# Optimization experiments

Hardware: AMD Instinct MI355X
Metric: run time of the kernel (lower is better)

Reference implementation:

```python
import jax, jax.numpy as jnp
import numpy as np

B, S, HID = 2, 2048, 1024
NH = 16
HD = HID // NH  # 64
ROPE_BASE = 10000.0
NEG_INF = -1e9


def _rope_emb(seq_len):
    # emb = cat(sin, cos) over head_dim, shape [1, S, 1, HD]
    inv_freq = 1.0 / (ROPE_BASE ** (jnp.arange(0, HD, 2, dtype=jnp.float32) / HD))
    pos = jnp.arange(seq_len, dtype=jnp.float32)
    sincos = pos[:, None] * inv_freq[None, :]            # [S, HD/2]
    emb = jnp.concatenate([jnp.sin(sincos), jnp.cos(sincos)], axis=-1)  # [S, HD]
    return emb[None, :, None, :]


def _apply_rope(x, emb):
    # Faithful to the (quirky) torch code: cos = emb[..., 1::2], sin = emb[..., ::2]
    cos = emb[..., 1::2]
    sin = emb[..., ::2]
    xe = x[..., ::2]
    xo = x[..., 1::2]
    return jnp.concatenate([xe * cos - xo * sin, xe * sin + xo * cos], axis=-1)


def setup_inputs() -> dict:
    key = jax.random.key(0)
    ks = jax.random.split(key, 5)
    hidden_states = jax.random.normal(ks[0], (B, S, HID), dtype=jnp.float32)
    # causal additive mask, broadcast over batch/heads
    causal = jnp.tril(jnp.ones((S, S), dtype=bool))
    attention_mask = jnp.where(causal, 0.0, NEG_INF).astype(jnp.float32)[None, None]
    scale = 1.0 / np.sqrt(HID)
    w_q = jax.random.normal(ks[1], (HID, HID), dtype=jnp.float32) * scale
    w_k = jax.random.normal(ks[2], (HID, HID), dtype=jnp.float32) * scale
    w_v = jax.random.normal(ks[3], (HID, HID), dtype=jnp.float32) * scale
    w_o = jax.random.normal(ks[4], (HID, HID), dtype=jnp.float32) * scale
    return {"hidden_states": hidden_states, "attention_mask": attention_mask,
            "w_q": w_q, "w_k": w_k, "w_v": w_v, "w_o": w_o}


def reference(hidden_states, attention_mask, w_q, w_k, w_v, w_o):
    b, s, _ = hidden_states.shape
    # torch Linear: x @ W.T (W is [out, in])
    q = (hidden_states @ w_q.T).reshape(b, s, NH, HD)
    k = (hidden_states @ w_k.T).reshape(b, s, NH, HD)
    v = (hidden_states @ w_v.T).reshape(b, s, NH, HD)
    emb = _rope_emb(s)
    q = _apply_rope(q, emb)
    k = _apply_rope(k, emb)
    # [b, h, s, d]
    q = q.transpose(0, 2, 1, 3)
    k = k.transpose(0, 2, 1, 3)
    v = v.transpose(0, 2, 1, 3)
    scores = jnp.einsum('bhqd,bhkd->bhqk', q, k) / np.sqrt(HD)
    scores = scores + attention_mask
    attn = jax.nn.softmax(scores, axis=-1)
    out = jnp.einsum('bhqk,bhkd->bhqd', attn, v)
    out = out.transpose(0, 2, 1, 3).reshape(b, s, HID)
    return out @ w_o.T
```

## Files before the change

### kernel.cpp

```cpp
#include <hip/hip_runtime.h>
#include <hip/hip_bf16.h>
#include <math.h>

typedef unsigned short u16;
typedef unsigned int   u32;
typedef unsigned long long u64;
typedef __attribute__((ext_vector_type(8))) short bf16x8;
typedef __attribute__((ext_vector_type(4))) short bf16x4;
typedef __attribute__((ext_vector_type(4))) float f32x4;

#define B_   2
#define S_   2048
#define HID_ 1024
#define NH_  16
#define HD_  64
#define MR_  (B_*S_)

#define QSCALE 0.1803368801111137f
#define MBIAS 32.0f

__device__ __forceinline__ u16 f2bf(float f) {
  union { float f; u32 u; } x; x.f = f;
  u32 r = x.u + 0x7fffu + ((x.u >> 16) & 1u);
  return (u16)(r >> 16);
}
__device__ __forceinline__ void gload16(const void* g, void* l) {
  __builtin_amdgcn_global_load_lds(
      (const __attribute__((address_space(1))) u32*)g,
      (__attribute__((address_space(3))) u32*)l, 16, 0, 0);
}

__global__ void k_cvt_all(const float* __restrict__ hs, const float* __restrict__ wq,
                          const float* __restrict__ wk, const float* __restrict__ wv,
                          const float* __restrict__ wo, ushort4* __restrict__ dst) {
  int i = blockIdx.x * blockDim.x + threadIdx.x;
  const float4* src;
  int idx;
  if (i < 1048576) {
    src = (const float4*)hs; idx = i;
  } else {
    int j = i - 1048576;
    int w = j >> 18; idx = j & 262143;
    src = (const float4*)(w == 0 ? wq : w == 1 ? wk : w == 2 ? wv : wo);
  }
  float4 v = src[idx];
  ushort4 o;
  o.x = f2bf(v.x); o.y = f2bf(v.y); o.z = f2bf(v.z); o.w = f2bf(v.w);
  dst[i] = o;
}

__global__ void k_rope_table(float2* __restrict__ tab) {
  int t = blockIdx.x * blockDim.x + threadIdx.x;
  int p = t >> 5, j = t & 31;
  double fp = (double)p;
  double c, s;
  if (j < 16) {
    s = sin(fp * pow(10000.0, -(2.0 * j) / 32.0));
    c = sin(fp * pow(10000.0, -(2.0 * j + 1.0) / 32.0));
  } else {
    s = cos(fp * pow(10000.0, -(2.0 * j - 32.0) / 32.0));
    c = cos(fp * pow(10000.0, -(2.0 * j - 31.0) / 32.0));
  }
  tab[p * 32 + j] = make_float2((float)c, (float)s);
}

__global__ __launch_bounds__(256) void k_qkv4(
    const u16* __restrict__ A,
    const u16* __restrict__ W0, const u16* __restrict__ W1, const u16* __restrict__ W2,
    u16* __restrict__ O0, u16* __restrict__ O1, u16* __restrict__ O2,
    const float2* __restrict__ tab) {
  __shared__ __align__(16) u16 Alds[2][2][128 * 32];
  __shared__ __align__(16) u16 Blds[2][2][128 * 32];

  int tid = threadIdx.x;
  int lane = tid & 63, wave = tid >> 6;
  int m0 = blockIdx.y * 128;
  int nt0 = blockIdx.x * 128;
  int wi = nt0 >> 10;
  const u16* W = (wi == 0) ? W0 : (wi == 1 ? W1 : W2);
  int n0 = nt0 & 1023;
  int wm = wave >> 1, wn = wave & 1;
  int lg = lane >> 4, lr = lane & 15;

  f32x4 acc[4][4];
  const f32x4 vz = {0.f, 0.f, 0.f, 0.f};
#pragma unroll
  for (int i = 0; i < 4; ++i)
#pragma unroll
    for (int j = 0; j < 4; ++j) acc[i][j] = vz;

  auto SA = [&](int j_, int d_, int hk_) {
#pragma unroll
    for (int it = 0; it < 2; ++it) {
      int c = it * 256 + tid;
      int row = c >> 2, sl = c & 3;
      int cw = sl ^ ((row >> 1) & 3);
      gload16(&A[(size_t)(m0 + row) * HID_ + j_ * 64 + hk_ * 32 + cw * 8],
              &Alds[d_][hk_][(it * 256 + wave * 64) * 8]);
    }
  };
  auto SB = [&](int j_, int d_, int hk_) {
#pragma unroll
    for (int it = 0; it < 2; ++it) {
      int c = it * 256 + tid;
      int row = c >> 2, sl = c & 3;
      int cw = sl ^ ((row >> 1) & 3);
      gload16(&W[(size_t)(n0 + row) * HID_ + j_ * 64 + hk_ * 32 + cw * 8],
              &Blds[d_][hk_][(it * 256 + wave * 64) * 8]);
    }
  };

  SA(0, 0, 0); SB(0, 0, 0); SA(0, 0, 1); SB(0, 0, 1);

  for (int j = 0; j < 16; ++j) {
    int cur = j & 1, nxt = cur ^ 1;
    bool more = (j < 15);
    bf16x8 bfr[4], afr[2];

    asm volatile("s_waitcnt vmcnt(4)" ::: "memory");
    __builtin_amdgcn_s_barrier();
    __builtin_amdgcn_sched_barrier(0);
    if (more) SA(j + 1, nxt, 0);
#pragma unroll
    for (int ni = 0; ni < 4; ++ni) {
      int row = wn * 64 + ni * 16 + lr;
      int ci = lg ^ ((row >> 1) & 3);
      bfr[ni] = *(const bf16x8*)&Blds[cur][0][row * 32 + ci * 8];
    }
#pragma unroll
    for (int mi = 0; mi < 2; ++mi) {
      int row = wm * 64 + mi * 16 + lr;
      int ci = lg ^ ((row >> 1) & 3);
      afr[mi] = *(const bf16x8*)&Alds[cur][0][row * 32 + ci * 8];
    }
    __builtin_amdgcn_s_setprio(1);
#pragma unroll
    for (int mi = 0; mi < 2; ++mi)
#pragma unroll
      for (int ni = 0; ni < 4; ++ni)
        acc[mi][ni] = __builtin_amdgcn_mfma_f32_16x16x32_bf16(afr[mi], bfr[ni], acc[mi][ni], 0, 0, 0);
    __builtin_amdgcn_s_setprio(0);

    if (more) SB(j + 1, nxt, 0);
#pragma unroll
    for (int mi = 0; mi < 2; ++mi) {
      int row = wm * 64 + (mi + 2) * 16 + lr;
      int ci = lg ^ ((row >> 1) & 3);
      afr[mi] = *(const bf16x8*)&Alds[cur][0][row * 32 + ci * 8];
    }
    __builtin_amdgcn_s_setprio(1);
#pragma unroll
    for (int mi = 0; mi < 2; ++mi)
#pragma unroll
      for (int ni = 0; ni < 4; ++ni)
        acc[mi + 2][ni] = __builtin_amdgcn_mfma_f32_16x16x32_bf16(afr[mi], bfr[ni], acc[mi + 2][ni], 0, 0, 0);
    __builtin_amdgcn_s_setprio(0);

    if (more) { asm volatile("s_waitcnt vmcnt(4)" ::: "memory"); }
    else      { asm volatile("s_waitcnt vmcnt(0)" ::: "memory"); }
    __builtin_amdgcn_s_barrier();
    __builtin_amdgcn_sched_barrier(0);
    if (more) SA(j + 1, nxt, 1);
#pragma unroll
    for (int ni = 0; ni < 4; ++ni) {
      int row = wn * 64 + ni * 16 + lr;
      int ci = lg ^ ((row >> 1) & 3);
      bfr[ni] = *(const bf16x8*)&Blds[cur][1][row * 32 + ci * 8];
    }
#pragma unroll
    for (int mi = 0; mi < 2; ++mi) {
      int row = wm * 64 + mi * 16 + lr;
      int ci = lg ^ ((row >> 1) & 3);
      afr[mi] = *(const bf16x8*)&Alds[cur][1][row * 32 + ci * 8];
    }
    __builtin_amdgcn_s_setprio(1);
#pragma unroll
    for (int mi = 0; mi < 2; ++mi)
#pragma unroll
      for (int ni = 0; ni < 4; ++ni)
        acc[mi][ni] = __builtin_amdgcn_mfma_f32_16x16x32_bf16(afr[mi], bfr[ni], acc[mi][ni], 0, 0, 0);
    __builtin_amdgcn_s_setprio(0);

    if (more) SB(j + 1, nxt, 1);
#pragma unroll
    for (int mi = 0; mi < 2; ++mi) {
      int row = wm * 64 + (mi + 2) * 16 + lr;
      int ci = lg ^ ((row >> 1) & 3);
      afr[mi] = *(const bf16x8*)&Alds[cur][1][row * 32 + ci * 8];
    }
    __builtin_amdgcn_s_setprio(1);
#pragma unroll
    for (int mi = 0; mi < 2; ++mi)
#pragma unroll
      for (int ni = 0; ni < 4; ++ni)
        acc[mi + 2][ni] = __builtin_amdgcn_mfma_f32_16x16x32_bf16(afr[mi], bfr[ni], acc[mi + 2][ni], 0, 0, 0);
    __builtin_amdgcn_s_setprio(0);
  }

  if (wi == 2) {
#pragma unroll
    for (int mi = 0; mi < 4; ++mi) {
      int grow0 = m0 + wm * 64 + mi * 16 + lg * 4;
      int bb = grow0 >> 11;
      int s = grow0 & 2047;
#pragma unroll
      for (int ni = 0; ni < 4; ++ni) {
        int gcol = n0 + wn * 64 + ni * 16 + lr;
        int h = gcol >> 6, dd = gcol & 63;
        u64 pk = (u64)f2bf(acc[mi][ni][0]) |
                 ((u64)f2bf(acc[mi][ni][1]) << 16) |
                 ((u64)f2bf(acc[mi][ni][2]) << 32) |
                 ((u64)f2bf(acc[mi][ni][3]) << 48);
        *(u64*)&O2[((size_t)(bb * NH_ + h) * HD_ + dd) * S_ + s] = pk;
      }
    }
  } else {
    u16* OB = wi ? O1 : O0;
    float sc = wi ? 1.0f : QSCALE;
#pragma unroll
    for (int mi = 0; mi < 4; ++mi) {
#pragma unroll
      for (int ni = 0; ni < 4; ++ni) {
        int gcol = n0 + wn * 64 + ni * 16 + lr;
        int h = gcol >> 6;
        int j = (gcol & 63) >> 1;
        bool even = !(gcol & 1);
        int ocol = h * 64 + (even ? j : 32 + j);
#pragma unroll
        for (int r = 0; r < 4; ++r) {
          float val = acc[mi][ni][r];
          float pv = __shfl_xor(val, 1);
          int grow = m0 + wm * 64 + mi * 16 + lg * 4 + r;
          int s = grow & 2047;
          float2 cs = tab[s * 32 + j];
          float xe = even ? val : pv;
          float xo = even ? pv : val;
          float res = even ? (xe * cs.x - xo * cs.y) : (xe * cs.y + xo * cs.x);
          OB[(size_t)grow * 1024 + ocol] = f2bf(res * sc);
        }
      }
    }
  }
}

__global__ __launch_bounds__(512) void k_oproj(
    const u16* __restrict__ A, const u16* __restrict__ W0,
    float* __restrict__ OF, int K) {
  __shared__ __align__(16) u16 Al[2][64 * 64];
  __shared__ __align__(16) u16 Bl[2][128 * 64];

  int tid = threadIdx.x;
  int lane = tid & 63, wave = tid >> 6;
  int m0 = blockIdx.y * 64;
  int n0 = blockIdx.x * 128;
  int wm = wave >> 1, wn = wave & 1;
  int lg = lane >> 4, lr = lane & 15;

  f32x4 acc[4];
  const f32x4 vz = {0.f, 0.f, 0.f, 0.f};
#pragma unroll
  for (int j = 0; j < 4; ++j) acc[j] = vz;

  auto STAGE = [&](int t_, int bs_) {
    int k0 = t_ * 64;
    {
      int c = tid;
      int row = c >> 3;
      int cw = (c & 7) ^ (row & 7);
      gload16(&A[(size_t)(m0 + row) * K + k0 + cw * 8], &Al[bs_][(wave * 64) * 8]);
    }
#pragma unroll
    for (int it = 0; it < 2; ++it) {
      int c = it * 512 + tid;
      int row = c >> 3;
      int cw = (c & 7) ^ (row & 7);
      gload16(&W0[(size_t)(n0 + row) * K + k0 + cw * 8], &Bl[bs_][(it * 512 + wave * 64) * 8]);
    }
  };

  int nkt = K >> 6;
  STAGE(0, 0);

  for (int t = 0; t < nkt; ++t) {
    int cur = t & 1;
    asm volatile("s_waitcnt vmcnt(0)" ::: "memory");
    __builtin_amdgcn_s_barrier();
    __builtin_amdgcn_sched_barrier(0);
    if (t + 1 < nkt) STAGE(t + 1, cur ^ 1);

#pragma unroll
    for (int kk = 0; kk < 2; ++kk) {
      bf16x8 af, bfr[4];
      {
        int row = wm * 16 + lr;
        int ci = (kk * 4 + lg) ^ (row & 7);
        af = *(const bf16x8*)&Al[cur][row * 64 + ci * 8];
      }
#pragma unroll
      for (int ni = 0; ni < 4; ++ni) {
        int row = wn * 64 + ni * 16 + lr;
        int ci = (kk * 4 + lg) ^ (row & 7);
        bfr[ni] = *(const bf16x8*)&Bl[cur][row * 64 + ci * 8];
      }
      __builtin_amdgcn_s_setprio(1);
#pragma unroll
      for (int ni = 0; ni < 4; ++ni)
        acc[ni] = __builtin_amdgcn_mfma_f32_16x16x32_bf16(af, bfr[ni], acc[ni], 0, 0, 0);
      __builtin_amdgcn_s_setprio(0);
    }
  }

#pragma unroll
  for (int ni = 0; ni < 4; ++ni)
#pragma unroll
    for (int r = 0; r < 4; ++r) {
      int grow = m0 + wm * 16 + lg * 4 + r;
      int gcol = n0 + wn * 64 + ni * 16 + lr;
      OF[(size_t)grow * 1024 + gcol] = acc[ni][r];
    }
}

__global__ __launch_bounds__(256, 4) void k_attn(
    const u16* __restrict__ Q, const u16* __restrict__ Kr, const u16* __restrict__ VT,
    u16* __restrict__ O) {
  __shared__ __align__(16) u16 Kl[2][64 * 64];
  __shared__ __align__(16) u16 Vl[2][64 * 64];

  int tid = threadIdx.x, lane = tid & 63, wave = tid >> 6;
  int id = blockIdx.x;
  int qt = 31 - (id >> 5);
  int bh = id & 31;
  int b = bh >> 4, h = bh & 15;
  int lg = lane >> 4, lr = lane & 15;
  int bS = b * S_;
  int nkt = qt + 1;
  int q0 = qt * 64 + wave * 16;

  const u16* vtb = &VT[(size_t)bh * HD_ * S_];
  int l8 = lane >> 3, l7 = lane & 7;
  int sl = l7 ^ l8;

  auto STAGE = [&](int kt_, int bs_) {
#pragma unroll
    for (int it = 0; it < 2; ++it) {
      int rb = wave * 16 + it * 8;
      int r = rb + l8;
      gload16(&Kr[(size_t)(bS + kt_ * 64 + r) * HID_ + h * HD_ + sl * 8],
              &Kl[bs_][rb * 64]);
      gload16(&vtb[(size_t)r * S_ + kt_ * 64 + sl * 8],
              &Vl[bs_][rb * 64]);
    }
  };

  STAGE(0, 0);

  bf16x8 qf[2];
#pragma unroll
  for (int kk = 0; kk < 2; ++kk)
    qf[kk] = *(const bf16x8*)
        &Q[(size_t)(bS + q0 + lr) * HID_ + h * HD_ + kk * 32 + lg * 8];

  f32x4 acc[4];
  const f32x4 vz = {0.f, 0.f, 0.f, 0.f};
#pragma unroll
  for (int df = 0; df < 4; ++df) acc[df] = vz;
  float l_ = 0.f;

  for (int kt = 0; kt < nkt; ++kt) {
    int cur = kt & 1;
    asm volatile("s_waitcnt vmcnt(0)" ::: "memory");
    __builtin_amdgcn_s_barrier();
    __builtin_amdgcn_sched_barrier(0);
    if (kt + 1 < nkt) STAGE(kt + 1, cur ^ 1);

    bf16x8 kfr[4][2];
#pragma unroll
    for (int kf = 0; kf < 4; ++kf) {
      int row = kf * 16 + lr;
#pragma unroll
      for (int kk = 0; kk < 2; ++kk) {
        int ci = (kk * 4 + lg) ^ (row & 7);
        kfr[kf][kk] = *(const bf16x8*)&Kl[cur][row * 64 + ci * 8];
      }
    }

    f32x4 st[4];
#pragma unroll
    for (int kf = 0; kf < 4; ++kf) st[kf] = vz;
    __builtin_amdgcn_s_setprio(1);
#pragma unroll
    for (int kk = 0; kk < 2; ++kk)
#pragma unroll
      for (int kf = 0; kf < 4; ++kf)
        st[kf] = __builtin_amdgcn_mfma_f32_16x16x32_bf16(
            kfr[kf][kk], qf[kk], st[kf], 0, 0, 0);
    __builtin_amdgcn_s_setprio(0);

    if (kt == qt) {
      int qg = q0 + lr;
#pragma unroll
      for (int kf = 0; kf < 4; ++kf)
#pragma unroll
        for (int r = 0; r < 4; ++r) {
          int kg = kt * 64 + kf * 16 + lg * 4 + r;
          if (kg > qg) st[kf][r] = -1e30f;
        }
    }

    float ts = 0.f;
    bf16x4 pb[4];
#pragma unroll
    for (int kf = 0; kf < 4; ++kf) {
#pragma unroll
      for (int r = 0; r < 4; ++r) {
        float e = __builtin_amdgcn_exp2f(st[kf][r] - MBIAS);
        st[kf][r] = e;
        ts += e;
      }
      u32 w0, w1;
      asm("v_cvt_pk_bf16_f32 %0, %1, %2" : "=v"(w0) : "v"(st[kf][0]), "v"(st[kf][1]));
      asm("v_cvt_pk_bf16_f32 %0, %1, %2" : "=v"(w1) : "v"(st[kf][2]), "v"(st[kf][3]));
      union { u32 u[2]; bf16x4 v; } pk;
      pk.u[0] = w0; pk.u[1] = w1;
      pb[kf] = pk.v;
    }
    l_ += ts;

    __builtin_amdgcn_s_setprio(1);
#pragma unroll
    for (int df = 0; df < 4; ++df) {
      int row = df * 16 + lr;
#pragma unroll
      for (int kf = 0; kf < 4; ++kf) {
        int slot = (kf * 2 + (lg >> 1)) ^ (row & 7);
        bf16x4 vfr = *(const bf16x4*)&Vl[cur][row * 64 + slot * 8 + (lg & 1) * 4];
        acc[df] = __builtin_amdgcn_mfma_f32_16x16x16bf16_1k(
            vfr, pb[kf], acc[df], 0, 0, 0);
      }
    }
    __builtin_amdgcn_s_setprio(0);
  }

  l_ += __shfl_xor(l_, 16);
  l_ += __shfl_xor(l_, 32);
  float inv = 1.0f / l_;
  int grow = bS + q0 + lr;
#pragma unroll
  for (int df = 0; df < 4; ++df) {
    u64 pk = (u64)f2bf(acc[df][0] * inv) |
             ((u64)f2bf(acc[df][1] * inv) << 16) |
             ((u64)f2bf(acc[df][2] * inv) << 32) |
             ((u64)f2bf(acc[df][3] * inv) << 48);
    *(u64*)&O[(size_t)grow * HID_ + h * HD_ + df * 16 + lg * 4] = pk;
  }
}

extern "C" void kernel_launch(void* const* d_in, const int* in_sizes, int n_in,
                              void* d_out, int out_size, void* d_ws, size_t ws_size,
                              hipStream_t stream) {
  const float* hs = (const float*)d_in[0];
  const float* wq = (const float*)d_in[2];
  const float* wk = (const float*)d_in[3];
  const float* wv = (const float*)d_in[4];
  const float* wo = (const float*)d_in[5];
  float* out = (float*)d_out;

  char* ws = (char*)d_ws;
  const size_t P = (size_t)MR_ * HID_ * 2;
  u16* Xb  = (u16*)(ws);
  u16* Wqb = (u16*)(ws + P);
  u16* Wkb = (u16*)(ws + P + (size_t)HID_ * HID_ * 2);
  u16* Wvb = (u16*)(ws + P + (size_t)HID_ * HID_ * 4);
  u16* Wob = (u16*)(ws + P + (size_t)HID_ * HID_ * 6);
  u16* q_r = (u16*)(ws + 2 * P);
  u16* k_r = (u16*)(ws + 3 * P);
  u16* vt  = (u16*)(ws + 4 * P);
  float2* tab = (float2*)(ws + 5 * P);
  u16* attn_o = Xb;

  k_cvt_all<<<8192, 256, 0, stream>>>(hs, wq, wk, wv, wo, (ushort4*)ws);
  k_rope_table<<<256, 256, 0, stream>>>(tab);

  k_qkv4<<<dim3(24, 32), 256, 0, stream>>>(
      Xb, Wqb, Wkb, Wvb, q_r, k_r, vt, tab);

  k_attn<<<1024, 256, 0, stream>>>(q_r, k_r, vt, attn_o);

  k_oproj<<<dim3(8, 64), 512, 0, stream>>>(attn_o, Wob, out, HID_);
}
```

Before: 129.4 us.

## Split QKV GEMM tile across eight waves and reorder attention prefetch

The QKV projection kernel now runs with 512 threads per block. Each of the eight waves owns a 32-row by 64-column slice instead of 64 by 64, which halves the per-wave accumulators and loads A and B with one load each per half-step. The attention kernel now issues the next K/V tile prefetch before waiting on the current one, and adds a trailing barrier so the buffer is not overwritten while still being read. This trades more waves per block and an extra barrier per iteration for higher occupancy and better overlap of loads with compute.

```diff
diff --git a/kernel.cpp b/kernel.cpp
--- a/kernel.cpp
+++ b/kernel.cpp
@@ -64,7 +64,7 @@
   tab[p * 32 + j] = make_float2((float)c, (float)s);
 }
 
-__global__ __launch_bounds__(256) void k_qkv4(
+__global__ __launch_bounds__(512) void k_qkv(
     const u16* __restrict__ A,
     const u16* __restrict__ W0, const u16* __restrict__ W1, const u16* __restrict__ W2,
     u16* __restrict__ O0, u16* __restrict__ O1, u16* __restrict__ O2,
@@ -82,45 +82,37 @@
   int wm = wave >> 1, wn = wave & 1;
   int lg = lane >> 4, lr = lane & 15;
 
-  f32x4 acc[4][4];
+  f32x4 acc[2][4];
   const f32x4 vz = {0.f, 0.f, 0.f, 0.f};
 #pragma unroll
-  for (int i = 0; i < 4; ++i)
+  for (int i = 0; i < 2; ++i)
 #pragma unroll
     for (int j = 0; j < 4; ++j) acc[i][j] = vz;
 
-  auto SA = [&](int j_, int d_, int hk_) {
-#pragma unroll
-    for (int it = 0; it < 2; ++it) {
-      int c = it * 256 + tid;
-      int row = c >> 2, sl = c & 3;
-      int cw = sl ^ ((row >> 1) & 3);
-      gload16(&A[(size_t)(m0 + row) * HID_ + j_ * 64 + hk_ * 32 + cw * 8],
-              &Alds[d_][hk_][(it * 256 + wave * 64) * 8]);
-    }
+  auto SA = [&](int t_, int d_, int hk_) {
+    int row = tid >> 2, sl = tid & 3;
+    int cw = sl ^ ((row >> 1) & 3);
+    gload16(&A[(size_t)(m0 + row) * HID_ + t_ * 64 + hk_ * 32 + cw * 8],
+            &Alds[d_][hk_][(wave * 64) * 8]);
   };
-  auto SB = [&](int j_, int d_, int hk_) {
-#pragma unroll
-    for (int it = 0; it < 2; ++it) {
-      int c = it * 256 + tid;
-      int row = c >> 2, sl = c & 3;
-      int cw = sl ^ ((row >> 1) & 3);
-      gload16(&W[(size_t)(n0 + row) * HID_ + j_ * 64 + hk_ * 32 + cw * 8],
-              &Blds[d_][hk_][(it * 256 + wave * 64) * 8]);
-    }
+  auto SB = [&](int t_, int d_, int hk_) {
+    int row = tid >> 2, sl = tid & 3;
+    int cw = sl ^ ((row >> 1) & 3);
+    gload16(&W[(size_t)(n0 + row) * HID_ + t_ * 64 + hk_ * 32 + cw * 8],
+            &Blds[d_][hk_][(wave * 64) * 8]);
   };
 
   SA(0, 0, 0); SB(0, 0, 0); SA(0, 0, 1); SB(0, 0, 1);
 
-  for (int j = 0; j < 16; ++j) {
-    int cur = j & 1, nxt = cur ^ 1;
-    bool more = (j < 15);
+  for (int t = 0; t < 16; ++t) {
+    int cur = t & 1, nxt = cur ^ 1;
+    bool more = (t < 15);
     bf16x8 bfr[4], afr[2];
 
-    asm volatile("s_waitcnt vmcnt(4)" ::: "memory");
+    asm volatile("s_waitcnt vmcnt(2)" ::: "memory");
     __builtin_amdgcn_s_barrier();
     __builtin_amdgcn_sched_barrier(0);
-    if (more) SA(j + 1, nxt, 0);
+    if (more) { SA(t + 1, nxt, 0); SB(t + 1, nxt, 0); }
 #pragma unroll
     for (int ni = 0; ni < 4; ++ni) {
       int row = wn * 64 + ni * 16 + lr;
@@ -129,7 +121,7 @@
     }
 #pragma unroll
     for (int mi = 0; mi < 2; ++mi) {
-      int row = wm * 64 + mi * 16 + lr;
+      int row = wm * 32 + mi * 16 + lr;
       int ci = lg ^ ((row >> 1) & 3);
       afr[mi] = *(const bf16x8*)&Alds[cur][0][row * 32 + ci * 8];
     }
@@ -141,26 +133,11 @@
         acc[mi][ni] = __builtin_amdgcn_mfma_f32_16x16x32_bf16(afr[mi], bfr[ni], acc[mi][ni], 0, 0, 0);
     __builtin_amdgcn_s_setprio(0);
 
-    if (more) SB(j + 1, nxt, 0);
-#pragma unroll
-    for (int mi = 0; mi < 2; ++mi) {
-      int row = wm * 64 + (mi + 2) * 16 + lr;
-      int ci = lg ^ ((row >> 1) & 3);
-      afr[mi] = *(const bf16x8*)&Alds[cur][0][row * 32 + ci * 8];
-    }
-    __builtin_amdgcn_s_setprio(1);
-#pragma unroll
-    for (int mi = 0; mi < 2; ++mi)
-#pragma unroll
-      for (int ni = 0; ni < 4; ++ni)
-        acc[mi + 2][ni] = __builtin_amdgcn_mfma_f32_16x16x32_bf16(afr[mi], bfr[ni], acc[mi + 2][ni], 0, 0, 0);
-    __builtin_amdgcn_s_setprio(0);
-
-    if (more) { asm volatile("s_waitcnt vmcnt(4)" ::: "memory"); }
+    if (more) { asm volatile("s_waitcnt vmcnt(2)" ::: "memory"); }
     else      { asm volatile("s_waitcnt vmcnt(0)" ::: "memory"); }
     __builtin_amdgcn_s_barrier();
     __builtin_amdgcn_sched_barrier(0);
-    if (more) SA(j + 1, nxt, 1);
+    if (more) { SA(t + 1, nxt, 1); SB(t + 1, nxt, 1); }
 #pragma unroll
     for (int ni = 0; ni < 4; ++ni) {
       int row = wn * 64 + ni * 16 + lr;
@@ -169,7 +146,7 @@
     }
 #pragma unroll
     for (int mi = 0; mi < 2; ++mi) {
-      int row = wm * 64 + mi * 16 + lr;
+      int row = wm * 32 + mi * 16 + lr;
       int ci = lg ^ ((row >> 1) & 3);
       afr[mi] = *(const bf16x8*)&Alds[cur][1][row * 32 + ci * 8];
     }
@@ -180,27 +157,12 @@
       for (int ni = 0; ni < 4; ++ni)
         acc[mi][ni] = __builtin_amdgcn_mfma_f32_16x16x32_bf16(afr[mi], bfr[ni], acc[mi][ni], 0, 0, 0);
     __builtin_amdgcn_s_setprio(0);
-
-    if (more) SB(j + 1, nxt, 1);
+  }
+
+  if (wi == 2) {
 #pragma unroll
     for (int mi = 0; mi < 2; ++mi) {
-      int row = wm * 64 + (mi + 2) * 16 + lr;
-      int ci = lg ^ ((row >> 1) & 3);
-      afr[mi] = *(const bf16x8*)&Alds[cur][1][row * 32 + ci * 8];
-    }
-    __builtin_amdgcn_s_setprio(1);
-#pragma unroll
-    for (int mi = 0; mi < 2; ++mi)
-#pragma unroll
-      for (int ni = 0; ni < 4; ++ni)
-        acc[mi + 2][ni] = __builtin_amdgcn_mfma_f32_16x16x32_bf16(afr[mi], bfr[ni], acc[mi + 2][ni], 0, 0, 0);
-    __builtin_amdgcn_s_setprio(0);
-  }
-
-  if (wi == 2) {
-#pragma unroll
-    for (int mi = 0; mi < 4; ++mi) {
-      int grow0 = m0 + wm * 64 + mi * 16 + lg * 4;
+      int grow0 = m0 + wm * 32 + mi * 16 + lg * 4;
       int bb = grow0 >> 11;
       int s = grow0 & 2047;
 #pragma unroll
@@ -218,7 +180,7 @@
     u16* OB = wi ? O1 : O0;
     float sc = wi ? 1.0f : QSCALE;
 #pragma unroll
-    for (int mi = 0; mi < 4; ++mi) {
+    for (int mi = 0; mi < 2; ++mi) {
 #pragma unroll
       for (int ni = 0; ni < 4; ++ni) {
         int gcol = n0 + wn * 64 + ni * 16 + lr;
@@ -230,7 +192,7 @@
         for (int r = 0; r < 4; ++r) {
           float val = acc[mi][ni][r];
           float pv = __shfl_xor(val, 1);
-          int grow = m0 + wm * 64 + mi * 16 + lg * 4 + r;
+          int grow = m0 + wm * 32 + mi * 16 + lg * 4 + r;
           int s = grow & 2047;
           float2 cs = tab[s * 32 + j];
           float xe = even ? val : pv;
@@ -368,10 +330,14 @@
 
   for (int kt = 0; kt < nkt; ++kt) {
     int cur = kt & 1;
-    asm volatile("s_waitcnt vmcnt(0)" ::: "memory");
+    if (kt + 1 < nkt) {
+      STAGE(kt + 1, cur ^ 1);
+      asm volatile("s_waitcnt vmcnt(4)" ::: "memory");
+    } else {
+      asm volatile("s_waitcnt vmcnt(0)" ::: "memory");
+    }
     __builtin_amdgcn_s_barrier();
     __builtin_amdgcn_sched_barrier(0);
-    if (kt + 1 < nkt) STAGE(kt + 1, cur ^ 1);
 
     bf16x8 kfr[4][2];
 #pragma unroll
@@ -439,6 +405,9 @@
       }
     }
     __builtin_amdgcn_s_setprio(0);
+
+    __builtin_amdgcn_sched_barrier(0);
+    __builtin_amdgcn_s_barrier();
   }
 
   l_ += __shfl_xor(l_, 16);
@@ -481,7 +450,7 @@
   k_cvt_all<<<8192, 256, 0, stream>>>(hs, wq, wk, wv, wo, (ushort4*)ws);
   k_rope_table<<<256, 256, 0, stream>>>(tab);
 
-  k_qkv4<<<dim3(24, 32), 256, 0, stream>>>(
+  k_qkv<<<dim3(24, 32), 512, 0, stream>>>(
       Xb, Wqb, Wkb, Wvb, q_r, k_r, vt, tab);
 
   k_attn<<<1024, 256, 0, stream>>>(q_r, k_r, vt, attn_o);
```

New measurement: 114.4 us, median of 2. 1.13x faster.
